# Optimization experiments

Hardware: AMD Instinct MI355X
Metric: run time of the kernel (lower is better)

The kernel has to match this reference:

```python
import jax, jax.numpy as jnp
from jax import lax
import numpy as np

D_MODEL = 512
MODES = 16
B, S = 8, 4096
EPS = 1e-5


def setup_inputs() -> dict:
    key = jax.random.key(0)
    ks = jax.random.split(key, 7)
    x = jax.random.normal(ks[0], (B, S, D_MODEL), dtype=jnp.float32)
    gamma = jnp.ones((D_MODEL,), dtype=jnp.float32)
    beta = jnp.zeros((D_MODEL,), dtype=jnp.float32)
    # complex spectral weights stored as real/imag parts, torch init: randn(cfloat)*0.02
    wr = jax.random.normal(ks[1], (D_MODEL, MODES), dtype=jnp.float32) * 0.02
    wi = jax.random.normal(ks[2], (D_MODEL, MODES), dtype=jnp.float32) * 0.02
    # Conv1d(d_model, d_model, 3): weight (out, in, k), torch default uniform(-b, b)
    bound = 1.0 / np.sqrt(D_MODEL * 3)
    conv_w = jax.random.uniform(ks[3], (D_MODEL, D_MODEL, 3), dtype=jnp.float32, minval=-bound, maxval=bound)
    conv_b = jax.random.uniform(ks[4], (D_MODEL,), dtype=jnp.float32, minval=-bound, maxval=bound)
    return {"x": x, "gamma": gamma, "beta": beta, "wr": wr, "wi": wi,
            "conv_w": conv_w, "conv_b": conv_b}


def reference(x, gamma, beta, wr, wi, conv_w, conv_b):
    Bq, Sq, Dq = x.shape
    residual = x
    # LayerNorm over last dim (biased variance, eps=1e-5)
    mu = jnp.mean(x, axis=-1, keepdims=True)
    var = jnp.var(x, axis=-1, keepdims=True)
    xn = (x - mu) * lax.rsqrt(var + EPS) * gamma + beta
    # truncated-mode spectral conv: rfft along seq, multiply first `modes` bins, irfft
    xf = jnp.fft.rfft(xn, axis=1, norm='ortho')           # [B, S//2+1, D] complex
    m = min(wr.shape[1], xf.shape[1])
    w = (wr + 1j * wi).T[:m]                              # [m, D]
    out_ft = jnp.zeros_like(xf).at[:, :m, :].set(xf[:, :m, :] * w[None])
    xs = jnp.fft.irfft(out_ft, n=Sq, axis=1, norm='ortho')  # [B, S, D] real
    # Conv1d(k=3, pad=1) over seq dim on channel-first layout
    xc = lax.conv_general_dilated(
        xs.transpose(0, 2, 1), conv_w, window_strides=(1,), padding=[(1, 1)],
        dimension_numbers=('NCH', 'OIH', 'NCH'))
    xc = (xc + conv_b[None, :, None]).transpose(0, 2, 1)
    return residual + xs + xc
```

## Files before the change

kernel.cpp:

```cpp
#include <hip/hip_runtime.h>
#include <hip/hip_bf16.h>
#include <math.h>

#define Bn 8
#define Sn 4096
#define Dn 512
#define MODES 16
#define ANGF 0.0015339807878856412f

#define PART_OFF 0
#define Y_OFF 8388608
#define WTF_OFF 8519680
#define Z_OFF 9306112

__global__ __launch_bounds__(256) void k_project(
    const float* __restrict__ x, const float* __restrict__ gamma,
    const float* __restrict__ beta, const float* __restrict__ cw,
    float* __restrict__ wTf, float* __restrict__ partials) {
  int blk = blockIdx.x;
  int tid = threadIdx.x;

  if (blk >= 512) {
    int base0 = (blk - 512) * 3072;
#pragma unroll
    for (int u = 0; u < 12; ++u) {
      int idx = base0 + (u << 8) + tid;
      int o = idx & 511;
      int d = (idx >> 9) & 511;
      int t = idx >> 18;
      wTf[idx] = cw[o * 1536 + d * 3 + t];
    }
    return;
  }

  int b = blk >> 6;
  int c = blk & 63;
  int d0 = tid << 1;
  int s_base = c << 4;

  __shared__ __attribute__((aligned(16))) float2 s_tw[16][MODES];
  __shared__ float2 s_mv[64];

  {
    int r = tid >> 4, k = tid & 15;
    int m = ((s_base + r) * k) & (Sn - 1);
    float sn, cn;
    __sincosf((float)m * ANGF, &sn, &cn);
    s_tw[r][k] = make_float2(cn, sn);
  }

  {
    int w = tid >> 6, lane = tid & 63;
    const float4* px = (const float4*)(
        x + (((size_t)((b << 12) + (w << 10) + s_base)) << 9));
#pragma unroll
    for (int rg = 0; rg < 16; rg += 4) {
      float4 v[8];
#pragma unroll
      for (int q = 0; q < 4; ++q) {
        v[2 * q] = px[(rg + q) * 128 + lane * 2];
        v[2 * q + 1] = px[(rg + q) * 128 + lane * 2 + 1];
      }
#pragma unroll
      for (int q = 0; q < 4; ++q) {
        float4 v0 = v[2 * q], v1 = v[2 * q + 1];
        float ps = v0.x + v0.y + v0.z + v0.w + v1.x + v1.y + v1.z + v1.w;
        float pq = v0.x * v0.x + v0.y * v0.y + v0.z * v0.z + v0.w * v0.w +
                   v1.x * v1.x + v1.y * v1.y + v1.z * v1.z + v1.w * v1.w;
#pragma unroll
        for (int off = 32; off > 0; off >>= 1) {
          ps += __shfl_down(ps, off);
          pq += __shfl_down(pq, off);
        }
        if (lane == 0) {
          float mu = ps * (1.0f / Dn);
          float var = pq * (1.0f / Dn) - mu * mu;
          s_mv[w * 16 + rg + q] = make_float2(mu, rsqrtf(var + 1e-5f));
        }
      }
    }
  }
  __syncthreads();

  float2 g = *(const float2*)(gamma + d0);
  float2 be = *(const float2*)(beta + d0);

  float2 accRe[MODES], accIm[MODES];
#pragma unroll
  for (int k = 0; k < MODES; k++) {
    accRe[k] = make_float2(0.f, 0.f);
    accIm[k] = make_float2(0.f, 0.f);
  }

  const float* xb = x + (((size_t)b << 12) << 9) + d0;
  float2 cur[4], nxt[4];
#pragma unroll
  for (int j = 0; j < 4; ++j)
    cur[j] = *(const float2*)(xb + ((size_t)((j << 10) + s_base) << 9));

#pragma unroll 2
  for (int r = 0; r < 16; ++r) {
    if (r < 15) {
#pragma unroll
      for (int j = 0; j < 4; ++j)
        nxt[j] =
            *(const float2*)(xb + ((size_t)((j << 10) + s_base + r + 1) << 9));
    }
    float2 xn[4];
#pragma unroll
    for (int j = 0; j < 4; ++j) {
      float2 mv = s_mv[(j << 4) + r];
      float ax = mv.y * g.x, ay = mv.y * g.y;
      xn[j] = make_float2((cur[j].x - mv.x) * ax + be.x,
                          (cur[j].y - mv.x) * ay + be.y);
    }
    float2 t02p = make_float2(xn[0].x + xn[2].x, xn[0].y + xn[2].y);
    float2 t02m = make_float2(xn[0].x - xn[2].x, xn[0].y - xn[2].y);
    float2 t13p = make_float2(xn[1].x + xn[3].x, xn[1].y + xn[3].y);
    float2 t13m = make_float2(xn[1].x - xn[3].x, xn[1].y - xn[3].y);
    float2 u0 = make_float2(t02p.x + t13p.x, t02p.y + t13p.y);
    float2 u1 = make_float2(t02p.x - t13p.x, t02p.y - t13p.y);

    const float4* twr = (const float4*)&s_tw[r][0];
#pragma unroll
    for (int kk = 0; kk < 8; ++kk) {
      float4 t2 = twr[kk];
      const int k0 = 2 * kk, k1 = 2 * kk + 1;
      {
        float2 u = ((k0 & 3) == 0) ? u0 : u1;
        accRe[k0].x += u.x * t2.x;
        accRe[k0].y += u.y * t2.x;
        accIm[k0].x -= u.x * t2.y;
        accIm[k0].y -= u.y * t2.y;
      }
      if ((k1 & 3) == 1) {
        accRe[k1].x += t2.z * t02m.x - t2.w * t13m.x;
        accRe[k1].y += t2.z * t02m.y - t2.w * t13m.y;
        accIm[k1].x -= t2.z * t13m.x + t2.w * t02m.x;
        accIm[k1].y -= t2.z * t13m.y + t2.w * t02m.y;
      } else {
        accRe[k1].x += t2.z * t02m.x + t2.w * t13m.x;
        accRe[k1].y += t2.z * t02m.y + t2.w * t13m.y;
        accIm[k1].x += t2.z * t13m.x - t2.w * t02m.x;
        accIm[k1].y += t2.z * t13m.y - t2.w * t02m.y;
      }
    }
#pragma unroll
    for (int j = 0; j < 4; ++j) cur[j] = nxt[j];
  }

  size_t base = ((size_t)(b * 64 + c)) * MODES;
  float4* P4 = (float4*)partials;
#pragma unroll
  for (int k = 0; k < MODES; k++)
    P4[(base + k) * 256 + tid] =
        make_float4(accRe[k].x, accIm[k].x, accRe[k].y, accIm[k].y);
}

__global__ __launch_bounds__(256) void k_reduce_modes(
    const float* __restrict__ partials, const float* __restrict__ wr,
    const float* __restrict__ wi, float* __restrict__ Y) {
  int idx = blockIdx.x * 256 + threadIdx.x;
  int d = idx & 511;
  int k = (idx >> 9) & 15;
  int b = idx >> 13;
  const float2* P = (const float2*)partials;
  float re = 0.f, im = 0.f;
#pragma unroll 8
  for (int c = 0; c < 64; c++) {
    float2 p = P[(((size_t)(b * 64 + c)) * MODES + k) * Dn + d];
    re += p.x;
    im += p.y;
  }
  float wrv = wr[d * MODES + k];
  float wiv = wi[d * MODES + k];
  float yre = re * wrv - im * wiv;
  float yim = re * wiv + im * wrv;
  float scale = (k == 0) ? (1.0f / 4096.0f) : (2.0f / 4096.0f);
  ((float2*)Y)[((size_t)b * MODES + k) * Dn + d] =
      make_float2(yre * scale, yim * scale);
}

__global__ __launch_bounds__(256) void k_build_z(
    const float* __restrict__ Y, const float* __restrict__ wTf,
    float* __restrict__ Z) {
  int blk = blockIdx.x;
  int b = blk / 24;
  int rem = blk % 24;
  int t = rem >> 3;
  int och = rem & 7;
  int tid = threadIdx.x;
  int oi = tid & 63, kq = tid >> 6;
  int o = och * 64 + oi;

  __shared__ float2 Ys[MODES][128];
  const float2* Y2 = (const float2*)Y;

  float zc[4] = {0.f, 0.f, 0.f, 0.f}, zs[4] = {0.f, 0.f, 0.f, 0.f};
  for (int dch = 0; dch < 4; ++dch) {
    int d0 = dch * 128;
#pragma unroll
    for (int i = 0; i < 8; i++) {
      int e = tid + i * 256;
      int k = e >> 7, dd = e & 127;
      Ys[k][dd] = Y2[(((size_t)(b * MODES + k)) << 9) + d0 + dd];
    }
    __syncthreads();

    const float* wp = wTf + (((size_t)(t * Dn + d0)) << 9) + o;
    float wv_n = wp[0];
    for (int dd = 0; dd < 128; ++dd) {
      float wv = wv_n;
      if (dd < 127) wv_n = wp[(size_t)(dd + 1) << 9];
#pragma unroll
      for (int m = 0; m < 4; m++) {
        float2 y = Ys[kq * 4 + m][dd];
        zc[m] += y.x * wv;
        zs[m] += y.y * wv;
      }
    }
    __syncthreads();
  }

  float2* Z2 = (float2*)Z;
#pragma unroll
  for (int m = 0; m < 4; m++) {
    int k = kq * 4 + m;
    Z2[(((size_t)((b * 3 + t) * MODES + k)) << 9) + o] =
        make_float2(zc[m], zs[m]);
  }
}

__global__ __launch_bounds__(256) void k_apply(
    const float* __restrict__ x, const float* __restrict__ Y,
    const float* __restrict__ Z, const float* __restrict__ conv_b,
    float* __restrict__ out) {
  int b = blockIdx.x >> 7;
  int rt = blockIdx.x & 127;
  int r0 = rt << 3;
  int tid = threadIdx.x;
  int o0 = tid << 1;

  __shared__ __attribute__((aligned(16))) float2 s_tw[8][MODES];
  if (tid < 128) {
    int rr = tid >> 4, k = tid & 15;
    int m = ((r0 + rr) * k) & (Sn - 1);
    float sn, cn;
    __sincosf((float)m * ANGF, &sn, &cn);
    s_tw[rr][k] = make_float2(cn, sn);
  }

  float2 Gc[MODES], Gs[MODES];
  float v0x = 0.f, v0y = 0.f, v1x = 0.f, v1y = 0.f;
  {
    const float4* Y4 = (const float4*)(Y + (((size_t)b * MODES) << 10));
    const float4* Z4 = (const float4*)(Z + (((size_t)b * 3 * MODES) << 10));
#pragma unroll
    for (int k = 0; k < MODES; k++) {
      float sf, cf;
      __sincosf((float)k * ANGF, &sf, &cf);
      float4 z0 = Z4[((0 * MODES + k) << 8) + tid];
      float4 z1 = Z4[((1 * MODES + k) << 8) + tid];
      float4 z2 = Z4[((2 * MODES + k) << 8) + tid];
      float4 y = Y4[(k << 8) + tid];
      float r0x = cf * z0.x + sf * z0.y;
      float i0x = cf * z0.y - sf * z0.x;
      float r2x = cf * z2.x - sf * z2.y;
      float i2x = cf * z2.y + sf * z2.x;
      Gc[k].x = y.x + r0x + z1.x + r2x;
      Gs[k].x = y.y + i0x + z1.y + i2x;
      float r0y = cf * z0.z + sf * z0.w;
      float i0y = cf * z0.w - sf * z0.z;
      float r2y = cf * z2.z - sf * z2.w;
      float i2y = cf * z2.w + sf * z2.z;
      Gc[k].y = y.z + r0y + z1.z + r2y;
      Gs[k].y = y.w + i0y + z1.w + i2y;
      v0x += r0x; v0y += r0y;
      v1x += z2.x; v1y += z2.z;
    }
  }
  float2 cb2 = *(const float2*)&conv_b[o0];
  __syncthreads();

  const float* xb = x + (((size_t)b << 12) << 9) + o0;
  float* ob = out + (((size_t)b << 12) << 9) + o0;

  float2 cur[4], nxt[4];
#pragma unroll
  for (int j = 0; j < 4; ++j)
    cur[j] = *(const float2*)(xb + ((size_t)((j << 10) + r0) << 9));

#pragma unroll 2
  for (int rr = 0; rr < 8; ++rr) {
    if (rr < 7) {
#pragma unroll
      for (int j = 0; j < 4; ++j)
        nxt[j] = *(const float2*)(xb + ((size_t)((j << 10) + r0 + rr + 1) << 9));
    }
    float2 a0 = make_float2(0.f, 0.f), a1 = a0, a2 = a0, a3 = a0;
    const float4* twr = (const float4*)&s_tw[rr][0];
#pragma unroll
    for (int kk = 0; kk < 8; ++kk) {
      float4 t2 = twr[kk];
#define APPLY_K(kidx, cc, ss)                                          \
  {                                                                    \
    float2 Pre = make_float2(cc * Gc[kidx].x - ss * Gs[kidx].x,        \
                             cc * Gc[kidx].y - ss * Gs[kidx].y);       \
    float2 Pim = make_float2(cc * Gs[kidx].x + ss * Gc[kidx].x,        \
                             cc * Gs[kidx].y + ss * Gc[kidx].y);       \
    a0.x += Pre.x; a0.y += Pre.y;                                      \
    if (((kidx) & 3) == 0) {                                           \
      a1.x += Pre.x; a1.y += Pre.y;                                    \
      a2.x += Pre.x; a2.y += Pre.y;                                    \
      a3.x += Pre.x; a3.y += Pre.y;                                    \
    } else if (((kidx) & 3) == 1) {                                    \
      a1.x -= Pim.x; a1.y -= Pim.y;                                    \
      a2.x -= Pre.x; a2.y -= Pre.y;                                    \
      a3.x += Pim.x; a3.y += Pim.y;                                    \
    } else if (((kidx) & 3) == 2) {                                    \
      a1.x -= Pre.x; a1.y -= Pre.y;                                    \
      a2.x += Pre.x; a2.y += Pre.y;                                    \
      a3.x -= Pre.x; a3.y -= Pre.y;                                    \
    } else {                                                           \
      a1.x += Pim.x; a1.y += Pim.y;                                    \
      a2.x -= Pre.x; a2.y -= Pre.y;                                    \
      a3.x -= Pim.x; a3.y -= Pim.y;                                    \
    }                                                                  \
  }
      APPLY_K(2 * kk, t2.x, t2.y);
      APPLY_K(2 * kk + 1, t2.z, t2.w);
#undef APPLY_K
    }
    int s_r = r0 + rr;
#pragma unroll
    for (int j = 0; j < 4; ++j) {
      float2 aj = (j == 0) ? a0 : (j == 1) ? a1 : (j == 2) ? a2 : a3;
      int s = s_r + (j << 10);
      float2 o2 = make_float2(cur[j].x + cb2.x + aj.x,
                              cur[j].y + cb2.y + aj.y);
      if (s == 0) { o2.x -= v0x; o2.y -= v0y; }
      if (s == Sn - 1) { o2.x -= v1x; o2.y -= v1y; }
      *(float2*)(ob + ((size_t)s << 9)) = o2;
    }
#pragma unroll
    for (int j = 0; j < 4; ++j) cur[j] = nxt[j];
  }
}

extern "C" void kernel_launch(void* const* d_in, const int* in_sizes, int n_in,
                              void* d_out, int out_size, void* d_ws,
                              size_t ws_size, hipStream_t stream) {
  const float* x = (const float*)d_in[0];
  const float* gamma = (const float*)d_in[1];
  const float* beta = (const float*)d_in[2];
  const float* wr = (const float*)d_in[3];
  const float* wi = (const float*)d_in[4];
  const float* conv_w = (const float*)d_in[5];
  const float* conv_b = (const float*)d_in[6];
  float* out = (float*)d_out;

  float* ws = (float*)d_ws;
  float* partials = ws + PART_OFF;
  float* Y = ws + Y_OFF;
  float* wTf = ws + WTF_OFF;
  float* Z = ws + Z_OFF;

  hipLaunchKernelGGL(k_project, dim3(768), dim3(256), 0, stream, x, gamma,
                     beta, conv_w, wTf, partials);
  hipLaunchKernelGGL(k_reduce_modes, dim3(256), dim3(256), 0, stream, partials,
                     wr, wi, Y);
  hipLaunchKernelGGL(k_build_z, dim3(192), dim3(256), 0, stream, Y, wTf, Z);
  hipLaunchKernelGGL(k_apply, dim3(1024), dim3(256), 0, stream, x, Y, Z,
                     conv_b, out);
}
```

Measured before the change: 206.0 us.

## Widen projection to one channel per thread and split build_z finer

k_project now runs 512 threads per block, each owning a single channel instead of a pair. It loads 16-row groups into two double-buffered register queues to overlap loads with the DFT accumulation, and halves the accumulator register footprint. k_build_z is reorganised so each thread computes one mode for one output channel, quadrupling the grid to 768 blocks, with padded shared memory and an unrolled inner loop. The intent is more parallelism and better latency hiding on both kernels. The cost is scalar float loads instead of float2, and more redundant Y staging per block in build_z.

```diff
diff --git a/kernel.cpp b/kernel.cpp
--- a/kernel.cpp
+++ b/kernel.cpp
@@ -13,7 +13,7 @@
 #define WTF_OFF 8519680
 #define Z_OFF 9306112
 
-__global__ __launch_bounds__(256) void k_project(
+__global__ __launch_bounds__(512) void k_project(
     const float* __restrict__ x, const float* __restrict__ gamma,
     const float* __restrict__ beta, const float* __restrict__ cw,
     float* __restrict__ wTf, float* __restrict__ partials) {
@@ -23,8 +23,8 @@
   if (blk >= 512) {
     int base0 = (blk - 512) * 3072;
 #pragma unroll
-    for (int u = 0; u < 12; ++u) {
-      int idx = base0 + (u << 8) + tid;
+    for (int u = 0; u < 6; ++u) {
+      int idx = base0 + (u << 9) + tid;
       int o = idx & 511;
       int d = (idx >> 9) & 511;
       int t = idx >> 18;
@@ -35,13 +35,13 @@
 
   int b = blk >> 6;
   int c = blk & 63;
-  int d0 = tid << 1;
   int s_base = c << 4;
+  int d = tid;
 
   __shared__ __attribute__((aligned(16))) float2 s_tw[16][MODES];
   __shared__ float2 s_mv[64];
 
-  {
+  if (tid < 256) {
     int r = tid >> 4, k = tid & 15;
     int m = ((s_base + r) * k) & (Sn - 1);
     float sn, cn;
@@ -51,15 +51,17 @@
 
   {
     int w = tid >> 6, lane = tid & 63;
-    const float4* px = (const float4*)(
-        x + (((size_t)((b << 12) + (w << 10) + s_base)) << 9));
-#pragma unroll
-    for (int rg = 0; rg < 16; rg += 4) {
+#pragma unroll
+    for (int eg = 0; eg < 8; eg += 4) {
       float4 v[8];
 #pragma unroll
       for (int q = 0; q < 4; ++q) {
-        v[2 * q] = px[(rg + q) * 128 + lane * 2];
-        v[2 * q + 1] = px[(rg + q) * 128 + lane * 2 + 1];
+        int e = w * 8 + eg + q;
+        int row = ((e >> 4) << 10) + s_base + (e & 15);
+        const float4* px =
+            (const float4*)(x + ((((size_t)(b << 12)) + row) << 9));
+        v[2 * q] = px[lane * 2];
+        v[2 * q + 1] = px[lane * 2 + 1];
       }
 #pragma unroll
       for (int q = 0; q < 4; ++q) {
@@ -75,86 +77,75 @@
         if (lane == 0) {
           float mu = ps * (1.0f / Dn);
           float var = pq * (1.0f / Dn) - mu * mu;
-          s_mv[w * 16 + rg + q] = make_float2(mu, rsqrtf(var + 1e-5f));
+          s_mv[w * 8 + eg + q] = make_float2(mu, rsqrtf(var + 1e-5f));
         }
       }
     }
   }
   __syncthreads();
 
-  float2 g = *(const float2*)(gamma + d0);
-  float2 be = *(const float2*)(beta + d0);
-
-  float2 accRe[MODES], accIm[MODES];
-#pragma unroll
-  for (int k = 0; k < MODES; k++) {
-    accRe[k] = make_float2(0.f, 0.f);
-    accIm[k] = make_float2(0.f, 0.f);
-  }
-
-  const float* xb = x + (((size_t)b << 12) << 9) + d0;
-  float2 cur[4], nxt[4];
-#pragma unroll
-  for (int j = 0; j < 4; ++j)
-    cur[j] = *(const float2*)(xb + ((size_t)((j << 10) + s_base) << 9));
-
-#pragma unroll 2
-  for (int r = 0; r < 16; ++r) {
-    if (r < 15) {
-#pragma unroll
-      for (int j = 0; j < 4; ++j)
-        nxt[j] =
-            *(const float2*)(xb + ((size_t)((j << 10) + s_base + r + 1) << 9));
-    }
-    float2 xn[4];
-#pragma unroll
-    for (int j = 0; j < 4; ++j) {
-      float2 mv = s_mv[(j << 4) + r];
-      float ax = mv.y * g.x, ay = mv.y * g.y;
-      xn[j] = make_float2((cur[j].x - mv.x) * ax + be.x,
-                          (cur[j].y - mv.x) * ay + be.y);
-    }
-    float2 t02p = make_float2(xn[0].x + xn[2].x, xn[0].y + xn[2].y);
-    float2 t02m = make_float2(xn[0].x - xn[2].x, xn[0].y - xn[2].y);
-    float2 t13p = make_float2(xn[1].x + xn[3].x, xn[1].y + xn[3].y);
-    float2 t13m = make_float2(xn[1].x - xn[3].x, xn[1].y - xn[3].y);
-    float2 u0 = make_float2(t02p.x + t13p.x, t02p.y + t13p.y);
-    float2 u1 = make_float2(t02p.x - t13p.x, t02p.y - t13p.y);
-
-    const float4* twr = (const float4*)&s_tw[r][0];
-#pragma unroll
-    for (int kk = 0; kk < 8; ++kk) {
-      float4 t2 = twr[kk];
-      const int k0 = 2 * kk, k1 = 2 * kk + 1;
-      {
-        float2 u = ((k0 & 3) == 0) ? u0 : u1;
-        accRe[k0].x += u.x * t2.x;
-        accRe[k0].y += u.y * t2.x;
-        accIm[k0].x -= u.x * t2.y;
-        accIm[k0].y -= u.y * t2.y;
-      }
-      if ((k1 & 3) == 1) {
-        accRe[k1].x += t2.z * t02m.x - t2.w * t13m.x;
-        accRe[k1].y += t2.z * t02m.y - t2.w * t13m.y;
-        accIm[k1].x -= t2.z * t13m.x + t2.w * t02m.x;
-        accIm[k1].y -= t2.z * t13m.y + t2.w * t02m.y;
-      } else {
-        accRe[k1].x += t2.z * t02m.x + t2.w * t13m.x;
-        accRe[k1].y += t2.z * t02m.y + t2.w * t13m.y;
-        accIm[k1].x += t2.z * t13m.x - t2.w * t02m.x;
-        accIm[k1].y += t2.z * t13m.y - t2.w * t02m.y;
-      }
-    }
-#pragma unroll
-    for (int j = 0; j < 4; ++j) cur[j] = nxt[j];
-  }
+  float g = gamma[d], be = beta[d];
+  float accRe[MODES], accIm[MODES];
+#pragma unroll
+  for (int k = 0; k < MODES; k++) { accRe[k] = 0.f; accIm[k] = 0.f; }
+
+  const float* xb = x + ((((size_t)(b << 12)) + s_base) << 9) + d;
+
+  float qA[16], qB[16];
+#define LOADQ(Q, RG)                                                      \
+  {                                                                       \
+    _Pragma("unroll") for (int j = 0; j < 4; ++j) {                       \
+      _Pragma("unroll") for (int rr = 0; rr < 4; ++rr) {                  \
+        Q[j * 4 + rr] = xb[(size_t)((j << 10) + (RG)*4 + rr) << 9];       \
+      }                                                                   \
+    }                                                                     \
+  }
+#define PROCQ(Q, RG)                                                      \
+  {                                                                       \
+    _Pragma("unroll") for (int rr = 0; rr < 4; ++rr) {                    \
+      int r = (RG)*4 + rr;                                                \
+      float xn[4];                                                        \
+      _Pragma("unroll") for (int j = 0; j < 4; ++j) {                     \
+        float2 mv = s_mv[(j << 4) + r];                                   \
+        xn[j] = (Q[j * 4 + rr] - mv.x) * (mv.y * g) + be;                 \
+      }                                                                   \
+      float t02p = xn[0] + xn[2], t02m = xn[0] - xn[2];                   \
+      float t13p = xn[1] + xn[3], t13m = xn[1] - xn[3];                   \
+      float u0 = t02p + t13p, u1 = t02p - t13p;                           \
+      const float4* twr = (const float4*)&s_tw[r][0];                     \
+      _Pragma("unroll") for (int kk = 0; kk < 8; ++kk) {                  \
+        float4 t2 = twr[kk];                                              \
+        const int k0 = 2 * kk, k1 = 2 * kk + 1;                           \
+        float u = ((k0 & 3) == 0) ? u0 : u1;                              \
+        accRe[k0] += u * t2.x;                                            \
+        accIm[k0] -= u * t2.y;                                            \
+        if ((k1 & 3) == 1) {    \
+          accRe[k1] += t2.z * t02m - t2.w * t13m;                         \
+          accIm[k1] -= t2.z * t13m + t2.w * t02m;                         \
+        } else {                           \
+          accRe[k1] += t2.z * t02m + t2.w * t13m;                         \
+          accIm[k1] += t2.z * t13m - t2.w * t02m;                         \
+        }                                                                 \
+      }                                                                   \
+    }                                                                     \
+  }
+
+  LOADQ(qA, 0);
+  LOADQ(qB, 1);
+  PROCQ(qA, 0);
+  LOADQ(qA, 2);
+  PROCQ(qB, 1);
+  LOADQ(qB, 3);
+  PROCQ(qA, 2);
+  PROCQ(qB, 3);
+#undef LOADQ
+#undef PROCQ
 
   size_t base = ((size_t)(b * 64 + c)) * MODES;
-  float4* P4 = (float4*)partials;
+  float2* P2 = (float2*)partials;
 #pragma unroll
   for (int k = 0; k < MODES; k++)
-    P4[(base + k) * 256 + tid] =
-        make_float4(accRe[k].x, accIm[k].x, accRe[k].y, accIm[k].y);
+    P2[(base + k) * Dn + d] = make_float2(accRe[k], accIm[k]);
 }
 
 __global__ __launch_bounds__(256) void k_reduce_modes(
@@ -185,50 +176,41 @@
     const float* __restrict__ Y, const float* __restrict__ wTf,
     float* __restrict__ Z) {
   int blk = blockIdx.x;
-  int b = blk / 24;
-  int rem = blk % 24;
-  int t = rem >> 3;
-  int och = rem & 7;
+  int b = blk / 96;
+  int rem = blk % 96;
+  int t = rem >> 5;
+  int och = rem & 31;
   int tid = threadIdx.x;
-  int oi = tid & 63, kq = tid >> 6;
-  int o = och * 64 + oi;
-
-  __shared__ float2 Ys[MODES][128];
+  int k = tid >> 4, oi = tid & 15;
+  int o = (och << 4) + oi;
+
+  __shared__ float2 Ys[MODES][129];
   const float2* Y2 = (const float2*)Y;
 
-  float zc[4] = {0.f, 0.f, 0.f, 0.f}, zs[4] = {0.f, 0.f, 0.f, 0.f};
+  float zc = 0.f, zs = 0.f;
   for (int dch = 0; dch < 4; ++dch) {
-    int d0 = dch * 128;
+    int d0 = dch << 7;
 #pragma unroll
     for (int i = 0; i < 8; i++) {
-      int e = tid + i * 256;
-      int k = e >> 7, dd = e & 127;
-      Ys[k][dd] = Y2[(((size_t)(b * MODES + k)) << 9) + d0 + dd];
+      int e = tid + (i << 8);
+      int kk = e >> 7, dd = e & 127;
+      Ys[kk][dd] = Y2[(((size_t)(b * MODES + kk)) << 9) + d0 + dd];
     }
     __syncthreads();
 
     const float* wp = wTf + (((size_t)(t * Dn + d0)) << 9) + o;
-    float wv_n = wp[0];
+#pragma unroll 8
     for (int dd = 0; dd < 128; ++dd) {
-      float wv = wv_n;
-      if (dd < 127) wv_n = wp[(size_t)(dd + 1) << 9];
-#pragma unroll
-      for (int m = 0; m < 4; m++) {
-        float2 y = Ys[kq * 4 + m][dd];
-        zc[m] += y.x * wv;
-        zs[m] += y.y * wv;
-      }
+      float wv = wp[(size_t)dd << 9];
+      float2 y = Ys[k][dd];
+      zc += y.x * wv;
+      zs += y.y * wv;
     }
     __syncthreads();
   }
 
-  float2* Z2 = (float2*)Z;
-#pragma unroll
-  for (int m = 0; m < 4; m++) {
-    int k = kq * 4 + m;
-    Z2[(((size_t)((b * 3 + t) * MODES + k)) << 9) + o] =
-        make_float2(zc[m], zs[m]);
-  }
+  ((float2*)Z)[(((size_t)((b * 3 + t) * MODES + k)) << 9) + o] =
+      make_float2(zc, zs);
 }
 
 __global__ __launch_bounds__(256) void k_apply(
@@ -365,11 +347,11 @@
   float* wTf = ws + WTF_OFF;
   float* Z = ws + Z_OFF;
 
-  hipLaunchKernelGGL(k_project, dim3(768), dim3(256), 0, stream, x, gamma,
+  hipLaunchKernelGGL(k_project, dim3(768), dim3(512), 0, stream, x, gamma,
                      beta, conv_w, wTf, partials);
   hipLaunchKernelGGL(k_reduce_modes, dim3(256), dim3(256), 0, stream, partials,
                      wr, wi, Y);
-  hipLaunchKernelGGL(k_build_z, dim3(192), dim3(256), 0, stream, Y, wTf, Z);
+  hipLaunchKernelGGL(k_build_z, dim3(768), dim3(256), 0, stream, Y, wTf, Z);
   hipLaunchKernelGGL(k_apply, dim3(1024), dim3(256), 0, stream, x, Y, Z,
                      conv_b, out);
 }
```

Result: slower. 269.7 us (+30.9%).

## Split LayerNorm stats into separate kernel and widen build_z parallelism

Applied to the files above, without the earlier changes.

Moves the per-row LayerNorm mean/rstd computation out of k_project into a new k_stats kernel that also does the conv weight transpose and writes stats to workspace. k_project then reads precomputed stats instead of re-reading 64 rows of x per block. k_build_z is restructured so each thread computes one (mode, output) pair, with 4x more blocks and a padded shared array, trading per-thread register reuse for more parallelism. The cost is an extra full pass over x (64 MB read) and an extra launch.

```diff
diff --git a/kernel.cpp b/kernel.cpp
--- a/kernel.cpp
+++ b/kernel.cpp
@@ -12,16 +12,17 @@
 #define Y_OFF 8388608
 #define WTF_OFF 8519680
 #define Z_OFF 9306112
-
-__global__ __launch_bounds__(256) void k_project(
-    const float* __restrict__ x, const float* __restrict__ gamma,
-    const float* __restrict__ beta, const float* __restrict__ cw,
-    float* __restrict__ wTf, float* __restrict__ partials) {
+#define STATS_OFF 9699328
+
+__global__ __launch_bounds__(256) void k_stats(const float* __restrict__ x,
+                                               const float* __restrict__ cw,
+                                               float* __restrict__ wTf,
+                                               float2* __restrict__ stats) {
   int blk = blockIdx.x;
   int tid = threadIdx.x;
 
-  if (blk >= 512) {
-    int base0 = (blk - 512) * 3072;
+  if (blk >= 1024) {
+    int base0 = (blk - 1024) * 3072;
 #pragma unroll
     for (int u = 0; u < 12; ++u) {
       int idx = base0 + (u << 8) + tid;
@@ -33,51 +34,50 @@
     return;
   }
 
+  int wave = tid >> 6, lane = tid & 63;
+  int row0 = blk * 32 + wave * 8;
+  for (int j = 0; j < 8; ++j) {
+    int row = row0 + j;
+    const float4* px = (const float4*)(x + ((size_t)row << 9));
+    float4 v0 = px[lane * 2];
+    float4 v1 = px[lane * 2 + 1];
+    float ps = v0.x + v0.y + v0.z + v0.w + v1.x + v1.y + v1.z + v1.w;
+    float pq = v0.x * v0.x + v0.y * v0.y + v0.z * v0.z + v0.w * v0.w +
+               v1.x * v1.x + v1.y * v1.y + v1.z * v1.z + v1.w * v1.w;
+#pragma unroll
+    for (int off = 32; off > 0; off >>= 1) {
+      ps += __shfl_down(ps, off);
+      pq += __shfl_down(pq, off);
+    }
+    if (lane == 0) {
+      float mu = ps * (1.0f / Dn);
+      float var = pq * (1.0f / Dn) - mu * mu;
+      stats[row] = make_float2(mu, rsqrtf(var + 1e-5f));
+    }
+  }
+}
+
+__global__ __launch_bounds__(256) void k_project(
+    const float* __restrict__ x, const float* __restrict__ gamma,
+    const float* __restrict__ beta, const float2* __restrict__ stats,
+    float* __restrict__ partials) {
+  int blk = blockIdx.x;
   int b = blk >> 6;
   int c = blk & 63;
+  int tid = threadIdx.x;
   int d0 = tid << 1;
   int s_base = c << 4;
 
   __shared__ __attribute__((aligned(16))) float2 s_tw[16][MODES];
   __shared__ float2 s_mv[64];
-
   {
     int r = tid >> 4, k = tid & 15;
     int m = ((s_base + r) * k) & (Sn - 1);
     float sn, cn;
     __sincosf((float)m * ANGF, &sn, &cn);
     s_tw[r][k] = make_float2(cn, sn);
-  }
-
-  {
-    int w = tid >> 6, lane = tid & 63;
-    const float4* px = (const float4*)(
-        x + (((size_t)((b << 12) + (w << 10) + s_base)) << 9));
-#pragma unroll
-    for (int rg = 0; rg < 16; rg += 4) {
-      float4 v[8];
-#pragma unroll
-      for (int q = 0; q < 4; ++q) {
-        v[2 * q] = px[(rg + q) * 128 + lane * 2];
-        v[2 * q + 1] = px[(rg + q) * 128 + lane * 2 + 1];
-      }
-#pragma unroll
-      for (int q = 0; q < 4; ++q) {
-        float4 v0 = v[2 * q], v1 = v[2 * q + 1];
-        float ps = v0.x + v0.y + v0.z + v0.w + v1.x + v1.y + v1.z + v1.w;
-        float pq = v0.x * v0.x + v0.y * v0.y + v0.z * v0.z + v0.w * v0.w +
-                   v1.x * v1.x + v1.y * v1.y + v1.z * v1.z + v1.w * v1.w;
-#pragma unroll
-        for (int off = 32; off > 0; off >>= 1) {
-          ps += __shfl_down(ps, off);
-          pq += __shfl_down(pq, off);
-        }
-        if (lane == 0) {
-          float mu = ps * (1.0f / Dn);
-          float var = pq * (1.0f / Dn) - mu * mu;
-          s_mv[w * 16 + rg + q] = make_float2(mu, rsqrtf(var + 1e-5f));
-        }
-      }
+    if (tid < 64) {
+      s_mv[tid] = stats[(b << 12) + ((tid >> 4) << 10) + s_base + (tid & 15)];
     }
   }
   __syncthreads();
@@ -185,50 +185,41 @@
     const float* __restrict__ Y, const float* __restrict__ wTf,
     float* __restrict__ Z) {
   int blk = blockIdx.x;
-  int b = blk / 24;
-  int rem = blk % 24;
-  int t = rem >> 3;
-  int och = rem & 7;
+  int b = blk / 96;
+  int rem = blk % 96;
+  int t = rem >> 5;
+  int och = rem & 31;
   int tid = threadIdx.x;
-  int oi = tid & 63, kq = tid >> 6;
-  int o = och * 64 + oi;
-
-  __shared__ float2 Ys[MODES][128];
+  int k = tid >> 4, oi = tid & 15;
+  int o = (och << 4) + oi;
+
+  __shared__ float2 Ys[MODES][129];
   const float2* Y2 = (const float2*)Y;
 
-  float zc[4] = {0.f, 0.f, 0.f, 0.f}, zs[4] = {0.f, 0.f, 0.f, 0.f};
+  float zc = 0.f, zs = 0.f;
   for (int dch = 0; dch < 4; ++dch) {
-    int d0 = dch * 128;
+    int d0 = dch << 7;
 #pragma unroll
     for (int i = 0; i < 8; i++) {
-      int e = tid + i * 256;
-      int k = e >> 7, dd = e & 127;
-      Ys[k][dd] = Y2[(((size_t)(b * MODES + k)) << 9) + d0 + dd];
+      int e = tid + (i << 8);
+      int kk = e >> 7, dd = e & 127;
+      Ys[kk][dd] = Y2[(((size_t)(b * MODES + kk)) << 9) + d0 + dd];
     }
     __syncthreads();
 
     const float* wp = wTf + (((size_t)(t * Dn + d0)) << 9) + o;
-    float wv_n = wp[0];
+#pragma unroll 8
     for (int dd = 0; dd < 128; ++dd) {
-      float wv = wv_n;
-      if (dd < 127) wv_n = wp[(size_t)(dd + 1) << 9];
-#pragma unroll
-      for (int m = 0; m < 4; m++) {
-        float2 y = Ys[kq * 4 + m][dd];
-        zc[m] += y.x * wv;
-        zs[m] += y.y * wv;
-      }
+      float wv = wp[(size_t)dd << 9];
+      float2 y = Ys[k][dd];
+      zc += y.x * wv;
+      zs += y.y * wv;
     }
     __syncthreads();
   }
 
-  float2* Z2 = (float2*)Z;
-#pragma unroll
-  for (int m = 0; m < 4; m++) {
-    int k = kq * 4 + m;
-    Z2[(((size_t)((b * 3 + t) * MODES + k)) << 9) + o] =
-        make_float2(zc[m], zs[m]);
-  }
+  ((float2*)Z)[(((size_t)((b * 3 + t) * MODES + k)) << 9) + o] =
+      make_float2(zc, zs);
 }
 
 __global__ __launch_bounds__(256) void k_apply(
@@ -364,12 +355,15 @@
   float* Y = ws + Y_OFF;
   float* wTf = ws + WTF_OFF;
   float* Z = ws + Z_OFF;
-
-  hipLaunchKernelGGL(k_project, dim3(768), dim3(256), 0, stream, x, gamma,
-                     beta, conv_w, wTf, partials);
+  float2* stats = (float2*)(ws + STATS_OFF);
+
+  hipLaunchKernelGGL(k_stats, dim3(1280), dim3(256), 0, stream, x, conv_w,
+                     wTf, stats);
+  hipLaunchKernelGGL(k_project, dim3(512), dim3(256), 0, stream, x, gamma,
+                     beta, stats, partials);
   hipLaunchKernelGGL(k_reduce_modes, dim3(256), dim3(256), 0, stream, partials,
                      wr, wi, Y);
-  hipLaunchKernelGGL(k_build_z, dim3(192), dim3(256), 0, stream, Y, wTf, Z);
+  hipLaunchKernelGGL(k_build_z, dim3(768), dim3(256), 0, stream, Y, wTf, Z);
   hipLaunchKernelGGL(k_apply, dim3(1024), dim3(256), 0, stream, x, Y, Z,
                      conv_b, out);
 }
```

Measured after the change: 206.6 us. Within noise of the previous version (+0.3%).
